# Optimization experiments

Hardware: AMD Instinct MI355X
Metric: run time of the kernel (lower is better)

## Reference

```python
import jax, jax.numpy as jnp
import numpy as np

PATCH = 8
EPS_LN = 1e-5
EPS_NORM = 1e-12


def conv1x1(x, w):
    # x: [b,i,h,w], w: [o,i]
    return jnp.einsum('bihw,oi->bohw', x, w)


def dwconv3(x, w):
    # depthwise 3x3, SAME padding; w: [C,1,3,3]
    return jax.lax.conv_general_dilated(
        x, w, window_strides=(1, 1), padding='SAME',
        feature_group_count=x.shape[1],
        dimension_numbers=('NCHW', 'OIHW', 'NCHW'))


def l2norm(x, axis=-1):
    n = jnp.sqrt(jnp.sum(x * x, axis=axis, keepdims=True))
    return x / jnp.maximum(n, EPS_NORM)


def layernorm_ch(x, w, b):
    # WithBias LayerNorm over the channel dim of NCHW (matches to_3d/to_4d)
    mu = jnp.mean(x, axis=1, keepdims=True)
    var = jnp.mean((x - mu) ** 2, axis=1, keepdims=True)
    return (x - mu) / jnp.sqrt(var + EPS_LN) * w[None, :, None, None] + b[None, :, None, None]


def patchify(t, p):
    b, c, h, w = t.shape
    t = t.reshape(b, c, h // p, p, w // p, p)
    return t.transpose(0, 1, 2, 4, 3, 5)  # b c gh gw p p


def unpatchify(t):
    b, c, gh, gw, p1, p2 = t.shape
    return t.transpose(0, 1, 2, 4, 3, 5).reshape(b, c, gh * p1, gw * p2)


def setup_inputs() -> dict:
    key = jax.random.key(0)
    ks = jax.random.split(key, 12)
    b, c, h, w = 4, 128, 256, 256
    heads = 8
    s = 0.05
    inp = {
        'x': jax.random.normal(ks[0], (b, c, h, w), jnp.float32),
        'qkv_w': s * jax.random.normal(ks[1], (3 * c, c), jnp.float32),
        'qkv_dw': s * jax.random.normal(ks[2], (3 * c, 1, 3, 3), jnp.float32),
        'proj_w': s * jax.random.normal(ks[3], (c, c), jnp.float32),
        'q1_w': s * jax.random.normal(ks[4], (c, c), jnp.float32),
        'q2_w': s * jax.random.normal(ks[5], (c, c), jnp.float32),
        'kv_w': s * jax.random.normal(ks[6], (2 * c, c), jnp.float32),
        'kv_dw': s * jax.random.normal(ks[7], (2 * c, 1, 3, 3), jnp.float32),
        'projf_w': s * jax.random.normal(ks[8], (c, c), jnp.float32),
        'temperature': jnp.ones((1, heads, 1, 1), jnp.float32),
        'ln_w': jnp.ones((c,), jnp.float32),
        'ln_b': jnp.zeros((c,), jnp.float32),
    }
    return inp


def reference(x, qkv_w, qkv_dw, proj_w, q1_w, q2_w, kv_w, kv_dw, projf_w,
              temperature, ln_w, ln_b):
    b, c, h, w = x.shape
    heads = temperature.shape[1]
    ch = c // heads

    # ---- channel (transposed) attention ----
    qkv = dwconv3(conv1x1(x, qkv_w), qkv_dw)
    q, k, v = jnp.split(qkv, 3, axis=1)
    q = l2norm(q.reshape(b, heads, ch, h * w))
    k = l2norm(k.reshape(b, heads, ch, h * w))
    v = v.reshape(b, heads, ch, h * w)
    attn = jax.nn.softmax(jnp.einsum('bhcn,bhdn->bhcd', q, k) * temperature, axis=-1)
    out = conv1x1(jnp.einsum('bhcd,bhdn->bhcn', attn, v).reshape(b, c, h, w), proj_w)

    # ---- FFT gating branch ----
    x_fft = jnp.fft.fftn(x, axes=(-2, -1)).real
    x_fft3 = conv1x1(jax.nn.gelu(conv1x1(x_fft, q1_w), approximate=False), q2_w)
    qf = jnp.fft.ifftn(x_fft3, axes=(-2, -1)).real

    kvf = dwconv3(conv1x1(out, kv_w), kv_dw)
    kf, vf = jnp.split(kvf, 2, axis=1)

    qp = patchify(vf, PATCH)  # note: original names vf's patches q_patch_1
    kp = patchify(kf, PATCH)
    prod = jnp.fft.rfft2(qp) * jnp.fft.rfft2(kp)
    out_1 = jnp.fft.irfft2(prod, s=(PATCH, PATCH))
    out_1 = unpatchify(out_1)
    out_1 = layernorm_ch(out_1, ln_w, ln_b) * qf
    return conv1x1(out_1, projf_w) + out
```

## Files before the change

### kernel.cpp

```cpp
#include <hip/hip_runtime.h>
#include <math.h>

#define HW 65536
#define CPX 64
#define XSTR 136

typedef short short8 __attribute__((ext_vector_type(8)));
typedef float f32x4 __attribute__((ext_vector_type(4)));

__device__ __forceinline__ float2 cmul(float2 a, float2 b){
  return make_float2(a.x*b.x - a.y*b.y, a.x*b.y + a.y*b.x);
}

__device__ __forceinline__ unsigned short f2bf(float f){
  unsigned u = __float_as_uint(f);
  u += 0x7fff + ((u >> 16) & 1);
  return (unsigned short)(u >> 16);
}
__device__ __forceinline__ float bf2f(unsigned short h){
  unsigned u = ((unsigned)h) << 16;
  return __uint_as_float(u);
}

__global__ __launch_bounds__(256,4) void conv1x1_mfma(
    const float* __restrict__ X, size_t bsX,
    const float* __restrict__ W, size_t bsW,
    float* __restrict__ Y, size_t bsY,
    const float* __restrict__ R, size_t bsR,
    int act)
{
  __shared__ __align__(16) unsigned short sbuf[2*CPX*XSTR];
  unsigned short* xh = sbuf;
  unsigned short* xl = sbuf + CPX*XSTR;
  const int t = threadIdx.x;
  const int l = t & 63;
  const int w = t >> 6;
  const int b = blockIdx.z;
  const int bx = ((blockIdx.x & 7) << 7) + (blockIdx.x >> 3);
  const size_t pxBase = (size_t)bx * CPX;
  const float* Xb = X + (size_t)b*bsX + pxBase;
  const float* Wb = W + (size_t)b*bsW;

  short8 whi[2][4], wlo[2][4];
  {
    const int row0 = (w<<5) + (l & 15);
    const int kg = (l >> 4) << 3;
    #pragma unroll
    for (int m=0;m<2;m++){
      #pragma unroll
      for (int ks=0;ks<4;ks++){
        const float* wp = Wb + (size_t)(row0 + 16*m)*128 + 32*ks + kg;
        float4 f0 = *(const float4*)wp;
        float4 f1 = *(const float4*)(wp+4);
        float fv[8] = {f0.x,f0.y,f0.z,f0.w,f1.x,f1.y,f1.z,f1.w};
        short8 h, lo;
        #pragma unroll
        for (int e=0;e<8;e++){
          unsigned short hb = f2bf(fv[e]);
          h[e]  = (short)hb;
          lo[e] = (short)f2bf(fv[e] - bf2f(hb));
        }
        whi[m][ks]=h; wlo[m][ks]=lo;
      }
    }
  }

  {
    const int px = (t & 15) << 2;
    const int s3 = (t & 7) << 3;
    #pragma unroll
    for (int i=0;i<8;i++){
      const int k = i*16 + (t >> 4);
      float4 v = *(const float4*)(Xb + (size_t)k*HW + px);
      const int kk = k ^ s3;
      float f[4] = {v.x,v.y,v.z,v.w};
      #pragma unroll
      for (int j=0;j<4;j++){
        unsigned short hb = f2bf(f[j]);
        xh[(px+j)*XSTR + kk] = hb;
        xl[(px+j)*XSTR + kk] = f2bf(f[j] - bf2f(hb));
      }
    }
  }
  __syncthreads();

  f32x4 acc[2][4];
  #pragma unroll
  for (int m=0;m<2;m++)
    #pragma unroll
    for (int n=0;n<4;n++) acc[m][n] = (f32x4){0.f,0.f,0.f,0.f};

  const int kg = (l>>4)<<3;
  #pragma unroll
  for (int ks=0;ks<4;ks++){
    const int k0 = 32*ks + kg;
    #pragma unroll
    for (int n=0;n<4;n++){
      const int px = 16*n + (l&15);
      const int off = px*XSTR + (k0 ^ (((px>>2)&7)<<3));
      short8 bh = *(short8*)&xh[off];
      short8 bl = *(short8*)&xl[off];
      #pragma unroll
      for (int m=0;m<2;m++){
        acc[m][n] = __builtin_amdgcn_mfma_f32_16x16x32_bf16(whi[m][ks], bh, acc[m][n], 0,0,0);
        acc[m][n] = __builtin_amdgcn_mfma_f32_16x16x32_bf16(wlo[m][ks], bh, acc[m][n], 0,0,0);
        acc[m][n] = __builtin_amdgcn_mfma_f32_16x16x32_bf16(whi[m][ks], bl, acc[m][n], 0,0,0);
      }
    }
  }
  __syncthreads();

  float* ost = (float*)sbuf;
  #pragma unroll
  for (int m=0;m<2;m++){
    const int ocb = (w<<5) + 16*m + ((l>>4)<<2);
    #pragma unroll
    for (int n=0;n<4;n++){
      const int px = 16*n + (l&15);
      #pragma unroll
      for (int r=0;r<4;r++){
        float v = acc[m][n][r];
        if (act==1) v = 0.5f*v*(1.f + erff(v*0.70710678118654752440f));
        ost[(ocb+r)*68 + px] = v;
      }
    }
  }
  __syncthreads();
  float* Yb = Y + (size_t)b*bsY + pxBase;
  const float* Rb = R ? (R + (size_t)b*bsR + pxBase) : 0;
  {
    const int px4 = (t & 15) << 2;
    #pragma unroll
    for (int it=0; it<8; it++){
      const int oc = it*16 + (t >> 4);
      float4 v4 = *(float4*)&ost[oc*68 + px4];
      if (Rb){
        float4 r4 = *(const float4*)(Rb + (size_t)oc*HW + px4);
        v4.x += r4.x; v4.y += r4.y; v4.z += r4.z; v4.w += r4.w;
      }
      *(float4*)(Yb + (size_t)oc*HW + px4) = v4;
    }
  }
}

__global__ __launch_bounds__(256,4) void dwconv3_row_k(
    const float* __restrict__ in, const float* __restrict__ w9,
    float* __restrict__ out, float* __restrict__ sqpart, int chOff)
{
  __shared__ float tl[34][256];
  int z = blockIdx.x;
  int cch = z & 127;
  int y0 = blockIdx.y * 32;
  size_t base = (size_t)z * HW;
  int t = threadIdx.x;
  float wv[9];
  #pragma unroll
  for (int i=0;i<9;i++) wv[i] = w9[cch*9+i];
  for (int idx = t; idx < 34*64; idx += 256){
    int r = idx >> 6, c4 = (idx & 63) << 2;
    int gy = y0 + r - 1;
    float4 v = make_float4(0.f,0.f,0.f,0.f);
    if ((unsigned)gy < 256u) v = *(const float4*)(in + base + (size_t)gy*256 + c4);
    *(float4*)&tl[r][c4] = v;
  }
  __syncthreads();
  const int ct = t;
  float ss = 0.f;
  for (int r = 0; r < 32; ++r){
    float acc = 0.f;
    #pragma unroll
    for (int dy=0; dy<3; dy++){
      float a  = (ct>0)   ? tl[r+dy][ct-1] : 0.f;
      float bm = tl[r+dy][ct];
      float c2 = (ct<255) ? tl[r+dy][ct+1] : 0.f;
      acc = fmaf(wv[dy*3+0], a, fmaf(wv[dy*3+1], bm, fmaf(wv[dy*3+2], c2, acc)));
    }
    out[base + (size_t)(y0+r)*256 + ct] = acc;
    ss += acc*acc;
  }
  if (sqpart){
    #pragma unroll
    for (int o=32;o>0;o>>=1) ss += __shfl_down(ss, o);
    __shared__ float red[4];
    if ((t&63)==0) red[t>>6] = ss;
    __syncthreads();
    if (t==0){
      float s = red[0]+red[1]+red[2]+red[3];
      int pg = ((z>>7)<<8) + chOff + cch;
      sqpart[pg*8 + blockIdx.y] = s;
    }
  }
}

__global__ __launch_bounds__(256) void qk_gram_k(
    const float* __restrict__ q, const float* __restrict__ k, float* __restrict__ Gp)
{
  __shared__ float qs[16][65], ks[16][65];
  int s = blockIdx.x, h = blockIdx.y, b = blockIdx.z;
  int t = threadIdx.x;
  int c = t >> 4, d = t & 15;
  const float* qb = q + ((size_t)b*128 + h*16)*HW + (size_t)s*1024;
  const float* kb = k + ((size_t)b*128 + h*16)*HW + (size_t)s*1024;
  float acc = 0.f;
  for (int n0=0;n0<1024;n0+=64){
    #pragma unroll
    for (int it=0;it<4;it++){
      int idx = it*256 + t;
      int row = idx >> 6, col = idx & 63;
      qs[row][col] = qb[(size_t)row*HW + n0 + col];
      ks[row][col] = kb[(size_t)row*HW + n0 + col];
    }
    __syncthreads();
    #pragma unroll
    for (int nn=0;nn<64;nn++) acc = fmaf(qs[c][nn], ks[d][nn], acc);
    __syncthreads();
  }
  Gp[(((size_t)b*8 + h)*64 + s)*256 + t] = acc;
}

__global__ __launch_bounds__(256) void attn_weff_k(
    const float* __restrict__ Gp, const float* __restrict__ sqpart,
    const float* __restrict__ temp, const float* __restrict__ proj_w,
    float* __restrict__ Weff)
{
  int b = blockIdx.x, t = threadIdx.x;
  __shared__ float G[8][16][16];
  __shared__ float A[8][16][16];
  __shared__ float rn_s[256];
  {
    const float* pp = sqpart + ((size_t)b*256 + t)*8;
    float s = 0.f;
    #pragma unroll
    for (int i=0;i<8;i++) s += pp[i];
    rn_s[t] = 1.f/fmaxf(sqrtf(s), 1e-12f);
  }
  __syncthreads();
  for (int e = t; e < 2048; e += 256){
    int h = e >> 8, cd = e & 255;
    int c = cd >> 4, d = cd & 15;
    const float* gp = Gp + (((size_t)b*8 + h)*64)*256 + cd;
    float sum = 0.f;
    for (int s2=0;s2<64;s2++) sum += gp[(size_t)s2*256];
    G[h][c][d] = sum * rn_s[h*16 + c] * rn_s[128 + h*16 + d] * temp[h];
  }
  __syncthreads();
  if (t < 128){
    int h = t >> 4, c = t & 15;
    float m = -1e30f;
    for (int d=0;d<16;d++) m = fmaxf(m, G[h][c][d]);
    float e[16], ssum = 0.f;
    for (int d=0;d<16;d++){ e[d] = expf(G[h][c][d]-m); ssum += e[d]; }
    float inv = 1.f/ssum;
    for (int d=0;d<16;d++) A[h][c][d] = e[d]*inv;
  }
  __syncthreads();
  for (int idx = t; idx < 16384; idx += 256){
    int o = idx >> 7, hd = idx & 127;
    int h = hd >> 4, d = hd & 15;
    float acc = 0.f;
    #pragma unroll
    for (int c=0;c<16;c++) acc = fmaf(proj_w[o*128 + h*16 + c], A[h][c][d], acc);
    Weff[((size_t)b*128 + o)*128 + hd] = acc;
  }
}

__global__ __launch_bounds__(256) void patch_circ_k(
    const float* __restrict__ vf, const float* __restrict__ kf, float* __restrict__ out)
{
  __shared__ float vs[8*260];
  __shared__ float ks2[8*260];
  size_t base = (size_t)blockIdx.y*HW + (size_t)blockIdx.x*2048;
  int t = threadIdx.x;
  #pragma unroll
  for (int it=0; it<2; it++){
    int idx = it*256 + t;
    int row = idx >> 6;
    int c4  = (idx & 63) << 2;
    float4 v  = *(const float4*)(vf + base + (size_t)row*256 + c4);
    float4 kv = *(const float4*)(kf + base + (size_t)row*256 + c4);
    *(float4*)&vs [row*260 + c4] = v;
    *(float4*)&ks2[row*260 + c4] = kv;
  }
  __syncthreads();
  int p = t & 31, pr = t >> 5;
  float acc[8];
  #pragma unroll
  for (int q=0;q<8;q++) acc[q]=0.f;
  #pragma unroll
  for (int i=0;i<8;i++){
    float4 va = *(float4*)&vs[i*260 + p*8];
    float4 vb = *(float4*)&vs[i*260 + p*8 + 4];
    int kr = (pr - i) & 7;
    float4 ka = *(float4*)&ks2[kr*260 + p*8];
    float4 kb = *(float4*)&ks2[kr*260 + p*8 + 4];
    float vv[8]={va.x,va.y,va.z,va.w,vb.x,vb.y,vb.z,vb.w};
    float kk[8]={ka.x,ka.y,ka.z,ka.w,kb.x,kb.y,kb.z,kb.w};
    #pragma unroll
    for (int q=0;q<8;q++)
      #pragma unroll
      for (int j=0;j<8;j++)
        acc[q] = fmaf(vv[j], kk[(q-j)&7], acc[q]);
  }
  float* op = out + base + (size_t)pr*256 + p*8;
  *(float4*)op     = make_float4(acc[0],acc[1],acc[2],acc[3]);
  *(float4*)(op+4) = make_float4(acc[4],acc[5],acc[6],acc[7]);
}

__global__ __launch_bounds__(64) void fft256_rows_r2c(
    const float* __restrict__ in, size_t inStride,
    float2* __restrict__ out, size_t outStride, float dir)
{
  __shared__ float2 buf[2][256];
  __shared__ float2 tw[128];
  int t = threadIdx.x;
  size_t row = blockIdx.x;
  const float* ip = in + (size_t)blockIdx.y*inStride + row*256;
  float2* op = out + (size_t)blockIdx.y*outStride + row*256;
  for (int i = t; i < 128; i += 64){
    float ang = 6.283185307179586477f * (float)i / 256.f;
    float s, c;
    sincosf(ang, &s, &c);
    tw[i] = make_float2(c, dir*s);
  }
  for (int i=t;i<256;i+=64) buf[0][i] = make_float2(ip[i], 0.f);
  int cur = 0, m = 1;
  for (int st=0; st<8; st++){
    __syncthreads();
    #pragma unroll
    for (int p2=0;p2<2;p2++){
      int bf = t + (p2<<6);
      int k = bf & (m-1);
      int jm = bf - k;
      float2 a = buf[cur][k + jm];
      float2 c = buf[cur][k + jm + 128];
      float2 w = tw[jm];
      float2 sm = make_float2(a.x+c.x, a.y+c.y);
      float2 df = make_float2(a.x-c.x, a.y-c.y);
      buf[cur^1][k + 2*jm]     = sm;
      buf[cur^1][k + 2*jm + m] = cmul(w, df);
    }
    cur ^= 1; m <<= 1;
  }
  __syncthreads();
  for (int i=t;i<256;i+=64) op[i] = buf[cur][i];
}

__global__ __launch_bounds__(256,4) void fft256_cols_c2r(
    const float2* __restrict__ in, size_t inStride,
    float* __restrict__ out, size_t outStride,
    float dir, float scale)
{
  __shared__ float2 buf[16*257];
  __shared__ float2 tw[128];
  const int t = threadIdx.x;
  const int col = t & 15, rr = t >> 4;
  const int cg0 = blockIdx.x << 4;
  const int plane = blockIdx.y;
  const float2* ip = in + (size_t)blockIdx.z*inStride + (size_t)plane*HW + cg0 + col;
  if (t < 128){
    float ang = 6.283185307179586477f * (float)t / 256.f;
    float s, c;
    sincosf(ang, &s, &c);
    tw[t] = make_float2(c, dir*s);
  }
  #pragma unroll
  for (int i=0;i<16;i++){
    int r = i*16 + rr;
    float2 v = ip[(size_t)r*256];
    int br = __brev((unsigned)r) >> 24;
    buf[col*257 + br] = v;
  }
  __syncthreads();
  for (int s=1;s<=8;s++){
    const int half = 1 << (s-1);
    const int tsh = 8 - s;
    #pragma unroll
    for (int j=0;j<8;j++){
      int bfi = rr + (j<<4);
      int lo = bfi & (half-1);
      int p  = ((bfi >> (s-1)) << s) + lo;
      float2 u = buf[col*257 + p];
      float2 v = buf[col*257 + p + half];
      float2 w = tw[lo << tsh];
      float2 wv = cmul(w, v);
      buf[col*257 + p]        = make_float2(u.x+wv.x, u.y+wv.y);
      buf[col*257 + p + half] = make_float2(u.x-wv.x, u.y-wv.y);
    }
    __syncthreads();
  }
  float* op = out + (size_t)blockIdx.z*outStride + (size_t)plane*HW + cg0;
  const int c0 = (t & 3) << 2;
  #pragma unroll
  for (int i=0;i<4;i++){
    int r = i*64 + (t >> 2);
    float4 o4 = make_float4(buf[(c0+0)*257 + r].x * scale,
                            buf[(c0+1)*257 + r].x * scale,
                            buf[(c0+2)*257 + r].x * scale,
                            buf[(c0+3)*257 + r].x * scale);
    *(float4*)(op + (size_t)r*256 + c0) = o4;
  }
}

__global__ __launch_bounds__(256) void ln_mul_k(
    const float* __restrict__ x, const float* __restrict__ qf,
    const float* __restrict__ lw, const float* __restrict__ lb,
    float* __restrict__ y)
{
  int b = blockIdx.y;
  size_t px0 = (size_t)blockIdx.x*64;
  int t = threadIdx.x;
  int px = t & 63, g = t >> 6;
  const float* xp = x + (size_t)b*8388608 + px0 + px;
  float vals[32];
  float s1 = 0.f, s2 = 0.f;
  #pragma unroll
  for (int i=0;i<32;i++){
    float v = xp[(size_t)(g*32+i)*HW];
    vals[i] = v; s1 += v; s2 += v*v;
  }
  __shared__ float r1[4][64], r2[4][64];
  r1[g][px] = s1; r2[g][px] = s2;
  __syncthreads();
  float S1 = r1[0][px]+r1[1][px]+r1[2][px]+r1[3][px];
  float S2 = r2[0][px]+r2[1][px]+r2[2][px]+r2[3][px];
  float mu = S1 * (1.f/128.f);
  float var = S2 * (1.f/128.f) - mu*mu;
  float rstd = rsqrtf(var + 1e-5f);
  const float* qp = qf + (size_t)b*8388608 + px0 + px;
  float* yp = y + (size_t)b*8388608 + px0 + px;
  #pragma unroll
  for (int i=0;i<32;i++){
    int c = g*32 + i;
    float v = (vals[i]-mu)*rstd*lw[c] + lb[c];
    yp[(size_t)c*HW] = v * qp[(size_t)c*HW];
  }
}

extern "C" void kernel_launch(void* const* d_in, const int* in_sizes, int n_in,
                              void* d_out, int out_size, void* d_ws, size_t ws_size,
                              hipStream_t stream)
{
  const float* x       = (const float*)d_in[0];
  const float* qkv_w   = (const float*)d_in[1];
  const float* qkv_dw  = (const float*)d_in[2];
  const float* proj_w  = (const float*)d_in[3];
  const float* q1_w    = (const float*)d_in[4];
  const float* q2_w    = (const float*)d_in[5];
  const float* kv_w    = (const float*)d_in[6];
  const float* kv_dw   = (const float*)d_in[7];
  const float* projf_w = (const float*)d_in[8];
  const float* temp    = (const float*)d_in[9];
  const float* ln_w    = (const float*)d_in[10];
  const float* ln_b    = (const float*)d_in[11];
  float* out = (float*)d_out;
  float* ws  = (float*)d_ws;

  const size_t P  = 33554432;
  const size_t CB = 8388608;
  const size_t CPLXB = 8388608;
  float* A = ws;
  float* B = ws + P;
  float* C = ws + 2*P;
  float* sqpart = ws + 3*P;
  float* Gp     = sqpart + 8192;
  float* Weff   = Gp + 524288;

  dim3 cg(1024,1,4); dim3 cb(256);
  dim3 dg(512,8);  dim3 db(256);

  conv1x1_mfma<<<cg,cb,0,stream>>>(x, CB, qkv_w + 0*16384, 0, A, CB, nullptr, 0, 0);
  dwconv3_row_k<<<dg,db,0,stream>>>(A, qkv_dw + 0*1152, out, sqpart, 0);
  conv1x1_mfma<<<cg,cb,0,stream>>>(x, CB, qkv_w + 1*16384, 0, B, CB, nullptr, 0, 0);
  dwconv3_row_k<<<dg,db,0,stream>>>(B, qkv_dw + 1*1152, A, sqpart, 128);
  qk_gram_k<<<dim3(64,8,4),256,0,stream>>>(out, A, Gp);
  attn_weff_k<<<4,256,0,stream>>>(Gp, sqpart, temp, proj_w, Weff);
  conv1x1_mfma<<<cg,cb,0,stream>>>(x, CB, qkv_w + 2*16384, 0, B, CB, nullptr, 0, 0);
  dwconv3_row_k<<<dg,db,0,stream>>>(B, qkv_dw + 2*1152, C, nullptr, 0);
  conv1x1_mfma<<<cg,cb,0,stream>>>(C, CB, Weff, 16384, B, CB, nullptr, 0, 0);
  conv1x1_mfma<<<cg,cb,0,stream>>>(B, CB, kv_w + 0*16384, 0, A, CB, nullptr, 0, 0);
  dwconv3_row_k<<<dg,db,0,stream>>>(A, kv_dw + 0*1152, out, nullptr, 0);
  conv1x1_mfma<<<cg,cb,0,stream>>>(B, CB, kv_w + 1*16384, 0, A, CB, nullptr, 0, 0);
  dwconv3_row_k<<<dg,db,0,stream>>>(A, kv_dw + 1*1152, C, nullptr, 0);
  patch_circ_k<<<dim3(32,512),256,0,stream>>>(C, out, A);
  for (int b=0;b<4;b+=2){
    fft256_rows_r2c<<<dim3(32768,2),64,0,stream>>>(x + (size_t)b*CB, CB, (float2*)C, CPLXB, -1.f);
    fft256_cols_c2r<<<dim3(16,128,2),256,0,stream>>>((const float2*)C, CPLXB, out + (size_t)b*CB, CB, -1.f, 1.f);
  }
  conv1x1_mfma<<<cg,cb,0,stream>>>(out, CB, q1_w, 0, C, CB, nullptr, 0, 1);
  conv1x1_mfma<<<cg,cb,0,stream>>>(C, CB, q2_w, 0, out, CB, nullptr, 0, 0);
  for (int b=0;b<4;b+=2){
    fft256_rows_r2c<<<dim3(32768,2),64,0,stream>>>(out + (size_t)b*CB, CB, (float2*)C, CPLXB, 1.f);
    fft256_cols_c2r<<<dim3(16,128,2),256,0,stream>>>((const float2*)C, CPLXB, out + (size_t)b*CB, CB, 1.f, 1.f/65536.f);
  }
  ln_mul_k<<<dim3(1024,4),256,0,stream>>>(A, out, ln_w, ln_b, C);
  conv1x1_mfma<<<cg,cb,0,stream>>>(C, CB, projf_w, 0, out, CB, B, CB, 0);
}
```

Before: 1.693 ms.

## Exploit Hermitian symmetry in real 2D FFTs and re-layout patch circulant shared memory

The row FFT now stores only the 129 non-redundant frequency bins per row. The column FFT runs on just those columns (9 blocks instead of 16) and writes the mirrored half of the real output using the conjugate-symmetry relation. This roughly halves the complex intermediate traffic and the column FFT work. Separately, the patch circulant kernel stores each patch contiguously in shared memory (stride 68) so per-thread float4 reads avoid bank conflicts. The symmetric write-back uses scattered scalar stores, which may partly offset the savings.

```diff
diff --git a/kernel.cpp b/kernel.cpp
--- a/kernel.cpp
+++ b/kernel.cpp
@@ -4,6 +4,7 @@
 #define HW 65536
 #define CPX 64
 #define XSTR 136
+#define RSTR 129
 
 typedef short short8 __attribute__((ext_vector_type(8)));
 typedef float f32x4 __attribute__((ext_vector_type(4)));
@@ -267,8 +268,8 @@
 __global__ __launch_bounds__(256) void patch_circ_k(
     const float* __restrict__ vf, const float* __restrict__ kf, float* __restrict__ out)
 {
-  __shared__ float vs[8*260];
-  __shared__ float ks2[8*260];
+  __shared__ float vs[32*68];
+  __shared__ float ks2[32*68];
   size_t base = (size_t)blockIdx.y*HW + (size_t)blockIdx.x*2048;
   int t = threadIdx.x;
   #pragma unroll
@@ -278,8 +279,9 @@
     int c4  = (idx & 63) << 2;
     float4 v  = *(const float4*)(vf + base + (size_t)row*256 + c4);
     float4 kv = *(const float4*)(kf + base + (size_t)row*256 + c4);
-    *(float4*)&vs [row*260 + c4] = v;
-    *(float4*)&ks2[row*260 + c4] = kv;
+    int p = c4 >> 3, j0 = c4 & 7;
+    *(float4*)&vs [p*68 + row*8 + j0] = v;
+    *(float4*)&ks2[p*68 + row*8 + j0] = kv;
   }
   __syncthreads();
   int p = t & 31, pr = t >> 5;
@@ -288,11 +290,11 @@
   for (int q=0;q<8;q++) acc[q]=0.f;
   #pragma unroll
   for (int i=0;i<8;i++){
-    float4 va = *(float4*)&vs[i*260 + p*8];
-    float4 vb = *(float4*)&vs[i*260 + p*8 + 4];
+    float4 va = *(float4*)&vs[p*68 + i*8];
+    float4 vb = *(float4*)&vs[p*68 + i*8 + 4];
     int kr = (pr - i) & 7;
-    float4 ka = *(float4*)&ks2[kr*260 + p*8];
-    float4 kb = *(float4*)&ks2[kr*260 + p*8 + 4];
+    float4 ka = *(float4*)&ks2[p*68 + kr*8];
+    float4 kb = *(float4*)&ks2[p*68 + kr*8 + 4];
     float vv[8]={va.x,va.y,va.z,va.w,vb.x,vb.y,vb.z,vb.w};
     float kk[8]={ka.x,ka.y,ka.z,ka.w,kb.x,kb.y,kb.z,kb.w};
     #pragma unroll
@@ -306,7 +308,7 @@
   *(float4*)(op+4) = make_float4(acc[4],acc[5],acc[6],acc[7]);
 }
 
-__global__ __launch_bounds__(64) void fft256_rows_r2c(
+__global__ __launch_bounds__(64) void fft256_rows_r2c_half(
     const float* __restrict__ in, size_t inStride,
     float2* __restrict__ out, size_t outStride, float dir)
 {
@@ -315,7 +317,7 @@
   int t = threadIdx.x;
   size_t row = blockIdx.x;
   const float* ip = in + (size_t)blockIdx.y*inStride + row*256;
-  float2* op = out + (size_t)blockIdx.y*outStride + row*256;
+  float2* op = out + (size_t)blockIdx.y*outStride + row*RSTR;
   for (int i = t; i < 128; i += 64){
     float ang = 6.283185307179586477f * (float)i / 256.f;
     float s, c;
@@ -342,10 +344,10 @@
     cur ^= 1; m <<= 1;
   }
   __syncthreads();
-  for (int i=t;i<256;i+=64) op[i] = buf[cur][i];
-}
-
-__global__ __launch_bounds__(256,4) void fft256_cols_c2r(
+  for (int i=t;i<256;i+=64) if (i <= 128) op[i] = buf[cur][i];
+}
+
+__global__ __launch_bounds__(256,4) void fft256_cols_c2r_herm(
     const float2* __restrict__ in, size_t inStride,
     float* __restrict__ out, size_t outStride,
     float dir, float scale)
@@ -354,9 +356,11 @@
   __shared__ float2 tw[128];
   const int t = threadIdx.x;
   const int col = t & 15, rr = t >> 4;
-  const int cg0 = blockIdx.x << 4;
+  const int u0 = blockIdx.x << 4;
+  const int u  = u0 + col;
   const int plane = blockIdx.y;
-  const float2* ip = in + (size_t)blockIdx.z*inStride + (size_t)plane*HW + cg0 + col;
+  const bool valid = (u <= 128);
+  const float2* ip = in + (size_t)blockIdx.z*inStride + (size_t)plane*(256*RSTR) + u;
   if (t < 128){
     float ang = 6.283185307179586477f * (float)t / 256.f;
     float s, c;
@@ -366,7 +370,7 @@
   #pragma unroll
   for (int i=0;i<16;i++){
     int r = i*16 + rr;
-    float2 v = ip[(size_t)r*256];
+    float2 v = valid ? ip[(size_t)r*RSTR] : make_float2(0.f,0.f);
     int br = __brev((unsigned)r) >> 24;
     buf[col*257 + br] = v;
   }
@@ -379,25 +383,40 @@
       int bfi = rr + (j<<4);
       int lo = bfi & (half-1);
       int p  = ((bfi >> (s-1)) << s) + lo;
-      float2 u = buf[col*257 + p];
-      float2 v = buf[col*257 + p + half];
-      float2 w = tw[lo << tsh];
-      float2 wv = cmul(w, v);
-      buf[col*257 + p]        = make_float2(u.x+wv.x, u.y+wv.y);
-      buf[col*257 + p + half] = make_float2(u.x-wv.x, u.y-wv.y);
+      float2 uq = buf[col*257 + p];
+      float2 vq = buf[col*257 + p + half];
+      float2 w  = tw[lo << tsh];
+      float2 wv = cmul(w, vq);
+      buf[col*257 + p]        = make_float2(uq.x+wv.x, uq.y+wv.y);
+      buf[col*257 + p + half] = make_float2(uq.x-wv.x, uq.y-wv.y);
     }
     __syncthreads();
   }
-  float* op = out + (size_t)blockIdx.z*outStride + (size_t)plane*HW + cg0;
-  const int c0 = (t & 3) << 2;
-  #pragma unroll
-  for (int i=0;i<4;i++){
-    int r = i*64 + (t >> 2);
-    float4 o4 = make_float4(buf[(c0+0)*257 + r].x * scale,
-                            buf[(c0+1)*257 + r].x * scale,
-                            buf[(c0+2)*257 + r].x * scale,
-                            buf[(c0+3)*257 + r].x * scale);
-    *(float4*)(op + (size_t)r*256 + c0) = o4;
+  float* op = out + (size_t)blockIdx.z*outStride + (size_t)plane*HW;
+  if (u0 < 128){
+    const int c0 = (t & 3) << 2;
+    #pragma unroll
+    for (int i=0;i<4;i++){
+      int r = i*64 + (t >> 2);
+      float4 o4 = make_float4(buf[(c0+0)*257 + r].x * scale,
+                              buf[(c0+1)*257 + r].x * scale,
+                              buf[(c0+2)*257 + r].x * scale,
+                              buf[(c0+3)*257 + r].x * scale);
+      *(float4*)(op + (size_t)r*256 + u0 + c0) = o4;
+    }
+    const int um = u0 + col;
+    if (um >= 1 && um <= 127){
+      const int mc = 256 - um;
+      #pragma unroll
+      for (int i=0;i<16;i++){
+        int r2 = i*16 + rr;
+        int src = (256 - r2) & 255;
+        op[(size_t)r2*256 + mc] = buf[col*257 + src].x * scale;
+      }
+    }
+  } else {
+    int r2 = t;
+    op[(size_t)r2*256 + 128] = buf[0*257 + r2].x * scale;
   }
 }
 
@@ -457,7 +476,7 @@
 
   const size_t P  = 33554432;
   const size_t CB = 8388608;
-  const size_t CPLXB = 8388608;
+  const size_t HSTR = 32768u*RSTR;
   float* A = ws;
   float* B = ws + P;
   float* C = ws + 2*P;
@@ -483,14 +502,14 @@
   dwconv3_row_k<<<dg,db,0,stream>>>(A, kv_dw + 1*1152, C, nullptr, 0);
   patch_circ_k<<<dim3(32,512),256,0,stream>>>(C, out, A);
   for (int b=0;b<4;b+=2){
-    fft256_rows_r2c<<<dim3(32768,2),64,0,stream>>>(x + (size_t)b*CB, CB, (float2*)C, CPLXB, -1.f);
-    fft256_cols_c2r<<<dim3(16,128,2),256,0,stream>>>((const float2*)C, CPLXB, out + (size_t)b*CB, CB, -1.f, 1.f);
+    fft256_rows_r2c_half<<<dim3(32768,2),64,0,stream>>>(x + (size_t)b*CB, CB, (float2*)C, HSTR, -1.f);
+    fft256_cols_c2r_herm<<<dim3(9,128,2),256,0,stream>>>((const float2*)C, HSTR, out + (size_t)b*CB, CB, -1.f, 1.f);
   }
   conv1x1_mfma<<<cg,cb,0,stream>>>(out, CB, q1_w, 0, C, CB, nullptr, 0, 1);
   conv1x1_mfma<<<cg,cb,0,stream>>>(C, CB, q2_w, 0, out, CB, nullptr, 0, 0);
   for (int b=0;b<4;b+=2){
-    fft256_rows_r2c<<<dim3(32768,2),64,0,stream>>>(out + (size_t)b*CB, CB, (float2*)C, CPLXB, 1.f);
-    fft256_cols_c2r<<<dim3(16,128,2),256,0,stream>>>((const float2*)C, CPLXB, out + (size_t)b*CB, CB, 1.f, 1.f/65536.f);
+    fft256_rows_r2c_half<<<dim3(32768,2),64,0,stream>>>(out + (size_t)b*CB, CB, (float2*)C, HSTR, 1.f);
+    fft256_cols_c2r_herm<<<dim3(9,128,2),256,0,stream>>>((const float2*)C, HSTR, out + (size_t)b*CB, CB, 1.f, 1.f/65536.f);
   }
   ln_mul_k<<<dim3(1024,4),256,0,stream>>>(A, out, ln_w, ln_b, C);
   conv1x1_mfma<<<cg,cb,0,stream>>>(C, CB, projf_w, 0, out, CB, B, CB, 0);
```

New measurement: 1.657 ms. -2.1%, faster.
